# Optimization experiments

Measured on AMD Instinct MI355X. Metric: run time of the kernel, lower is better.

Reference implementation:

```python
import jax, jax.numpy as jnp
import numpy as np

B, S, D = 4, 2048, 1024
H = 16
HD = D // H  # head_dim = 64


def setup_inputs() -> dict:
    key = jax.random.key(0)
    ks = jax.random.split(key, 8)
    scale = 1.0 / np.sqrt(D)
    return {
        "X_Q": jax.random.normal(ks[0], (B, S, D), dtype=jnp.float32),
        "X_KV": jax.random.normal(ks[1], (B, S, D), dtype=jnp.float32),
        # q_proj: Linear(D, D), weights stored as (in, out)
        "q_w": jax.random.normal(ks[2], (D, D), dtype=jnp.float32) * scale,
        "q_b": jax.random.normal(ks[3], (D,), dtype=jnp.float32) * scale,
        # kv_proj: Linear(D, 2*D)
        "kv_w": jax.random.normal(ks[4], (D, 2 * D), dtype=jnp.float32) * scale,
        "kv_b": jax.random.normal(ks[5], (2 * D,), dtype=jnp.float32) * scale,
        # out_proj: Linear(D, D) (query_dim == input_dim)
        "out_w": jax.random.normal(ks[6], (D, D), dtype=jnp.float32) * scale,
        "out_b": jax.random.normal(ks[7], (D,), dtype=jnp.float32) * scale,
    }


def reference(X_Q, X_KV, q_w, q_b, kv_w, kv_b, out_w, out_b):
    # projections
    q = X_Q @ q_w + q_b                      # [b, s, D]
    kv = X_KV @ kv_w + kv_b                  # [b, l, 2D]
    k, v = jnp.split(kv, 2, axis=-1)         # each [b, l, D]

    def split_heads(t):
        b, m, _ = t.shape
        return t.reshape(b, m, H, HD).transpose(0, 2, 1, 3)  # [b, h, m, d]

    q, k, v = split_heads(q), split_heads(k), split_heads(v)

    # standard attention: full SxL scores (non-flash path)
    scores = jnp.einsum("bhsd,bhld->bhsl", q, k) / np.sqrt(HD)
    attn = jax.nn.softmax(scores, axis=-1)   # dropout_p = 0 -> identity
    out = jnp.einsum("bhsl,bhld->bhsd", attn, v)

    # merge heads: [b, h, s, d] -> [b, s, h*d]
    out = out.transpose(0, 2, 1, 3).reshape(B, S, D)
    return out @ out_w + out_b
```

## Files before the change

### kernel.cpp

```cpp
#include <hip/hip_runtime.h>
#include <hip/hip_bf16.h>
#include <math.h>

#define B_  4
#define S_  2048
#define D_  1024
#define H_  16
#define HD_ 64

typedef __bf16 bf16;
typedef __bf16 bf16x4 __attribute__((ext_vector_type(4)));
typedef __bf16 bf16x8 __attribute__((ext_vector_type(8)));
typedef float  floatx4 __attribute__((ext_vector_type(4)));
typedef unsigned short ushort8 __attribute__((ext_vector_type(8)));

#define QSCALE 0.18033688011112042f

__device__ __forceinline__ void async_load16(const bf16* g, bf16* l) {
  __builtin_amdgcn_global_load_lds(
      (const __attribute__((address_space(1))) void*)g,
      (__attribute__((address_space(3))) void*)l, 16, 0, 0);
}

__global__ __launch_bounds__(256) void cast_both(
    const float* __restrict__ ina, bf16* __restrict__ outa,
    const float* __restrict__ inb, bf16* __restrict__ outb) {
  int bid = blockIdx.x;
  const float* in;
  bf16* out;
  int i;
  if (bid < 8192) { in = ina; out = outa; i = (bid * 256 + threadIdx.x) * 4; }
  else            { in = inb; out = outb; i = ((bid - 8192) * 256 + threadIdx.x) * 4; }
  float4 v = *reinterpret_cast<const float4*>(in + i);
  bf16x4 o;
  o[0] = (bf16)v.x; o[1] = (bf16)v.y; o[2] = (bf16)v.z; o[3] = (bf16)v.w;
  *reinterpret_cast<bf16x4*>(out + i) = o;
}

__global__ __launch_bounds__(256) void transcast_all(
    const float* __restrict__ qw, bf16* __restrict__ qwT,
    const float* __restrict__ kvw, bf16* __restrict__ kvwT,
    const float* __restrict__ ow, bf16* __restrict__ owT) {
  __shared__ float tile[32][33];
  int bid = blockIdx.x;
  const float* in; bf16* out; int N, lb;
  if (bid < 1024)      { in = qw;  out = qwT;  N = 1024; lb = bid; }
  else if (bid < 3072) { in = kvw; out = kvwT; N = 2048; lb = bid - 1024; }
  else                 { in = ow;  out = owT;  N = 1024; lb = bid - 3072; }
  int nx = N >> 5;
  int n0 = (lb % nx) * 32, k0 = (lb / nx) * 32;
  int tx = threadIdx.x & 31, ty = threadIdx.x >> 5;
  #pragma unroll
  for (int i = ty; i < 32; i += 8)
    tile[i][tx] = in[(size_t)(k0 + i) * N + n0 + tx];
  __syncthreads();
  #pragma unroll
  for (int i = ty; i < 32; i += 8)
    out[(size_t)(n0 + i) * 1024 + k0 + tx] = (bf16)tile[tx][i];
}

template <int MODE>
__global__ __launch_bounds__(256) void gemm_bt(
    const bf16* __restrict__ A, const bf16* __restrict__ Bt,
    const float* __restrict__ bias, void* __restrict__ out,
    int M, int N, int K) {
  __shared__ bf16 As[128][64];
  __shared__ bf16 Bs[128][64];

  const int tid  = threadIdx.x;
  const int m0   = blockIdx.y * 128;
  const int n0   = blockIdx.x * 128;
  const int w    = tid >> 6;
  const int lane = tid & 63;
  const int lr   = lane & 15;
  const int lq   = lane >> 4;
  const int wm   = (w >> 1) * 64;
  const int wn   = (w & 1) * 64;

  const int srow = lane >> 3;
  const int sg   = (lane & 7) ^ srow;
  const bf16* aptr = A  + (size_t)(m0 + 32 * w + srow) * K + 8 * sg;
  const bf16* bptr = Bt + (size_t)(n0 + 32 * w + srow) * K + 8 * sg;

  floatx4 acc[4][4];
  #pragma unroll
  for (int i = 0; i < 4; i++)
    #pragma unroll
    for (int j = 0; j < 4; j++)
      acc[i][j] = floatx4{0.f, 0.f, 0.f, 0.f};

  for (int k0 = 0; k0 < K; k0 += 64) {
    __syncthreads();
    #pragma unroll
    for (int p = 0; p < 4; p++) {
      async_load16(aptr + (size_t)8 * p * K + k0, &As[32 * w + 8 * p][0]);
      async_load16(bptr + (size_t)8 * p * K + k0, &Bs[32 * w + 8 * p][0]);
    }
    __syncthreads();
    #pragma unroll
    for (int kc = 0; kc < 2; kc++) {
      const int sw = 8 * ((kc * 4 + lq) ^ (lr & 7));
      bf16x8 af[4], bfv[4];
      #pragma unroll
      for (int t = 0; t < 4; t++)
        af[t] = *reinterpret_cast<const bf16x8*>(&As[wm + 16 * t + lr][sw]);
      #pragma unroll
      for (int t = 0; t < 4; t++)
        bfv[t] = *reinterpret_cast<const bf16x8*>(&Bs[wn + 16 * t + lr][sw]);
      #pragma unroll
      for (int i = 0; i < 4; i++)
        #pragma unroll
        for (int j = 0; j < 4; j++)
          acc[i][j] = __builtin_amdgcn_mfma_f32_16x16x32_bf16(af[i], bfv[j], acc[i][j], 0, 0, 0);
    }
  }

  #pragma unroll
  for (int i = 0; i < 4; i++) {
    int row_base = m0 + wm + 16 * i + lq * 4;
    #pragma unroll
    for (int j = 0; j < 4; j++) {
      int col = n0 + wn + 16 * j + lr;
      float bv = bias[col];
      if (MODE == 2 && col >= 1024) {
        int b = row_base >> 11, s0 = row_base & 2047;
        int c = col - 1024, h = c >> 6, d = c & 63;
        bf16* Vt = (bf16*)out + (size_t)B_ * H_ * S_ * HD_;
        bf16x4 pk;
        #pragma unroll
        for (int r = 0; r < 4; r++) pk[r] = (bf16)(acc[i][j][r] + bv);
        *reinterpret_cast<bf16x4*>(
            &Vt[(((size_t)b * H_ + h) * HD_ + d) * S_ + s0]) = pk;
        continue;
      }
      #pragma unroll
      for (int r = 0; r < 4; r++) {
        int row = row_base + r;
        float v = acc[i][j][r] + bv;
        if (MODE == 0) {
          ((float*)out)[(size_t)row * N + col] = v;
        } else if (MODE == 1) {
          int b = row >> 11, s = row & 2047;
          int h = col >> 6, d = col & 63;
          ((bf16*)out)[(((size_t)b * H_ + h) * S_ + s) * HD_ + d] =
              (bf16)(v * QSCALE);
        } else {
          int b = row >> 11, s = row & 2047;
          int h = col >> 6, d = col & 63;
          ((bf16*)out)[(((size_t)b * H_ + h) * S_ + s) * HD_ + d] = (bf16)v;
        }
      }
    }
  }
}

__global__ __launch_bounds__(256, 2) void attn_kernel(
    const bf16* __restrict__ Q, const bf16* __restrict__ Kb,
    const bf16* __restrict__ Vt, bf16* __restrict__ out) {
  __shared__ bf16 smem[32768];

  const int tid  = threadIdx.x;
  const int w    = tid >> 6;
  const int lane = tid & 63;
  const int lr   = lane & 15;
  const int lq   = lane >> 4;
  const int bh   = blockIdx.x;
  const int q0   = blockIdx.y * 256;
  const size_t base = (size_t)bh * S_ * HD_;

  bf16* pw = smem + 16384 + w * 4096;

  const int srow = lane >> 3;
  const int sg   = (lane & 7) ^ srow;

  const bf16* kptr = Kb + base + (size_t)(16 * w + srow) * HD_ + 8 * sg;
  const bf16* vptr = Vt + base + (size_t)(16 * w + srow) * S_  + 8 * sg;

  #pragma unroll
  for (int p = 0; p < 2; p++) {
    async_load16(kptr + (size_t)8 * p * HD_, smem + (16 * w + 8 * p) * 64);
    async_load16(vptr + (size_t)8 * p * S_,  smem + 4096 + (16 * w + 8 * p) * 64);
  }

  bf16x8 bq[4][2];
  #pragma unroll
  for (int g = 0; g < 4; g++) {
    const bf16* qrow = Q + base + (size_t)(q0 + 64 * w + 16 * g + lr) * HD_;
    bq[g][0] = *reinterpret_cast<const bf16x8*>(qrow + lq * 8);
    bq[g][1] = *reinterpret_cast<const bf16x8*>(qrow + 32 + lq * 8);
  }

  const int sw0 = 8 * ((0 + lq) ^ (lr & 7));
  const int sw1 = 8 * ((4 + lq) ^ (lr & 7));
  const int pcolbase = 4 * (lq & 1);
  const int pswz = lr & 7;

  float l_i[4] = {0.f, 0.f, 0.f, 0.f};
  floatx4 o_acc[4][4];
  #pragma unroll
  for (int g = 0; g < 4; g++)
    #pragma unroll
    for (int t = 0; t < 4; t++) o_acc[g][t] = floatx4{0.f, 0.f, 0.f, 0.f};

  __syncthreads();

  const int NIT = S_ / 64;
  for (int it = 0; it < NIT; it++) {
    bf16* ks  = smem + (it & 1) * 8192;
    bf16* vts = ks + 4096;

    if (it + 1 < NIT) {
      bf16* ksn = smem + ((it + 1) & 1) * 8192;
      const int l0n = (it + 1) * 64;
      #pragma unroll
      for (int p = 0; p < 2; p++) {
        async_load16(kptr + (size_t)(l0n + 8 * p) * HD_, ksn + (16 * w + 8 * p) * 64);
        async_load16(vptr + (size_t)8 * p * S_ + l0n,    ksn + 4096 + (16 * w + 8 * p) * 64);
      }
    }

    auto qkt = [&](int t) {
      bf16x8 ak0 = *reinterpret_cast<const bf16x8*>(ks + (16 * t + lr) * 64 + sw0);
      bf16x8 ak1 = *reinterpret_cast<const bf16x8*>(ks + (16 * t + lr) * 64 + sw1);
      floatx4 sc[4];
      #pragma unroll
      for (int g = 0; g < 4; g++) {
        sc[g] = __builtin_amdgcn_mfma_f32_16x16x32_bf16(ak0, bq[g][0],
                    floatx4{0.f, 0.f, 0.f, 0.f}, 0, 0, 0);
        sc[g] = __builtin_amdgcn_mfma_f32_16x16x32_bf16(ak1, bq[g][1], sc[g], 0, 0, 0);
      }
      const int pcol = 8 * ((2 * t + (lq >> 1)) ^ pswz) + pcolbase;
      #pragma unroll
      for (int g = 0; g < 4; g++) {
        bf16x4 pk;
        float lsum = 0.f;
        #pragma unroll
        for (int r = 0; r < 4; r++) {
          float p = __builtin_amdgcn_exp2f(sc[g][r]);
          lsum += p;
          pk[r] = (bf16)p;
        }
        l_i[g] += lsum;
        *reinterpret_cast<bf16x4*>(&pw[(16 * g + lr) * 64 + pcol]) = pk;
      }
    };

    qkt(0);
    qkt(1);
    __builtin_amdgcn_wave_barrier();

    {
      bf16x8 bp0[4], av0[4];
      #pragma unroll
      for (int g = 0; g < 4; g++)
        bp0[g] = *reinterpret_cast<const bf16x8*>(&pw[(16 * g + lr) * 64 + sw0]);
      #pragma unroll
      for (int t2 = 0; t2 < 4; t2++)
        av0[t2] = *reinterpret_cast<const bf16x8*>(vts + (16 * t2 + lr) * 64 + sw0);
      qkt(2);
      #pragma unroll
      for (int t2 = 0; t2 < 2; t2++)
        #pragma unroll
        for (int g = 0; g < 4; g++)
          o_acc[g][t2] = __builtin_amdgcn_mfma_f32_16x16x32_bf16(av0[t2], bp0[g], o_acc[g][t2], 0, 0, 0);
      qkt(3);
      #pragma unroll
      for (int t2 = 2; t2 < 4; t2++)
        #pragma unroll
        for (int g = 0; g < 4; g++)
          o_acc[g][t2] = __builtin_amdgcn_mfma_f32_16x16x32_bf16(av0[t2], bp0[g], o_acc[g][t2], 0, 0, 0);
    }
    __builtin_amdgcn_wave_barrier();

    {
      bf16x8 bp1[4];
      #pragma unroll
      for (int g = 0; g < 4; g++)
        bp1[g] = *reinterpret_cast<const bf16x8*>(&pw[(16 * g + lr) * 64 + sw1]);
      #pragma unroll
      for (int t2 = 0; t2 < 4; t2++) {
        bf16x8 av = *reinterpret_cast<const bf16x8*>(vts + (16 * t2 + lr) * 64 + sw1);
        #pragma unroll
        for (int g = 0; g < 4; g++)
          o_acc[g][t2] = __builtin_amdgcn_mfma_f32_16x16x32_bf16(av, bp1[g], o_acc[g][t2], 0, 0, 0);
      }
    }

    __syncthreads();
  }

  #pragma unroll
  for (int g = 0; g < 4; g++) {
    l_i[g] += __shfl_xor(l_i[g], 16, 64);
    l_i[g] += __shfl_xor(l_i[g], 32, 64);
  }

  const int b = bh >> 4, h = bh & 15;
  #pragma unroll
  for (int g = 0; g < 4; g++) {
    const float inv = 1.0f / l_i[g];
    const int qrow = q0 + 64 * w + 16 * g + lr;
    bf16* orow = out + ((size_t)b * S_ + qrow) * D_ + h * HD_;
    #pragma unroll
    for (int t = 0; t < 4; t++) {
      bf16x4 pk;
      #pragma unroll
      for (int r = 0; r < 4; r++) pk[r] = (bf16)(o_acc[g][t][r] * inv);
      *reinterpret_cast<bf16x4*>(&orow[16 * t + lq * 4]) = pk;
    }
  }
}

extern "C" void kernel_launch(void* const* d_in, const int* in_sizes, int n_in,
                              void* d_out, int out_size, void* d_ws, size_t ws_size,
                              hipStream_t stream) {
  const float* X_Q   = (const float*)d_in[0];
  const float* X_KV  = (const float*)d_in[1];
  const float* q_w   = (const float*)d_in[2];
  const float* q_b   = (const float*)d_in[3];
  const float* kv_w  = (const float*)d_in[4];
  const float* kv_b  = (const float*)d_in[5];
  const float* out_w = (const float*)d_in[6];
  const float* out_b = (const float*)d_in[7];
  float* out = (float*)d_out;

  char* ws = (char*)d_ws;
  const size_t MB = 1024 * 1024;
  bf16* Xq   = (bf16*)(ws + 0);
  bf16* Xkv  = (bf16*)(ws + 16 * MB);
  bf16* Qb   = (bf16*)(ws + 32 * MB);
  bf16* Kb   = (bf16*)(ws + 48 * MB);
  bf16* qwT  = (bf16*)(ws + 80 * MB);
  bf16* kvwT = (bf16*)(ws + 82 * MB);
  bf16* owT  = (bf16*)(ws + 86 * MB);
  bf16* Vt   = Kb + (size_t)B_ * H_ * S_ * HD_;
  bf16* attn = Xq;

  cast_both<<<16384, 256, 0, stream>>>(X_Q, Xq, X_KV, Xkv);
  transcast_all<<<4096, 256, 0, stream>>>(q_w, qwT, kv_w, kvwT, out_w, owT);

  gemm_bt<1><<<dim3(8, 64), 256, 0, stream>>>(Xq, qwT, q_b, Qb, 8192, 1024, 1024);
  gemm_bt<2><<<dim3(16, 64), 256, 0, stream>>>(Xkv, kvwT, kv_b, Kb, 8192, 2048, 1024);
  attn_kernel<<<dim3(64, 8), 256, 0, stream>>>(Qb, Kb, Vt, attn);
  gemm_bt<0><<<dim3(8, 64), 256, 0, stream>>>(attn, owT, out_b, out, 8192, 1024, 1024);
}
```

Measured before the change: 308.5 us.

## Merge Q and KV projection GEMMs into one launch, add MFMA priority hints

Result: no change. 309.0 us (+0.2%).

```diff
diff --git a/kernel.cpp b/kernel.cpp
--- a/kernel.cpp
+++ b/kernel.cpp
@@ -12,7 +12,6 @@
 typedef __bf16 bf16x4 __attribute__((ext_vector_type(4)));
 typedef __bf16 bf16x8 __attribute__((ext_vector_type(8)));
 typedef float  floatx4 __attribute__((ext_vector_type(4)));
-typedef unsigned short ushort8 __attribute__((ext_vector_type(8)));
 
 #define QSCALE 0.18033688011112042f
 
@@ -60,16 +59,14 @@
 }
 
 template <int MODE>
-__global__ __launch_bounds__(256) void gemm_bt(
+__device__ __forceinline__ void gemm_body(
     const bf16* __restrict__ A, const bf16* __restrict__ Bt,
     const float* __restrict__ bias, void* __restrict__ out,
-    int M, int N, int K) {
-  __shared__ bf16 As[128][64];
-  __shared__ bf16 Bs[128][64];
-
+    int M, int N, int K, int bx, int by,
+    bf16 (*As)[64], bf16 (*Bs)[64]) {
   const int tid  = threadIdx.x;
-  const int m0   = blockIdx.y * 128;
-  const int n0   = blockIdx.x * 128;
+  const int m0   = by * 128;
+  const int n0   = bx * 128;
   const int w    = tid >> 6;
   const int lane = tid & 63;
   const int lr   = lane & 15;
@@ -154,6 +151,31 @@
   }
 }
 
+__global__ __launch_bounds__(256) void gemm_out(
+    const bf16* __restrict__ A, const bf16* __restrict__ Bt,
+    const float* __restrict__ bias, void* __restrict__ out,
+    int M, int N, int K) {
+  __shared__ bf16 As[128][64];
+  __shared__ bf16 Bs[128][64];
+  gemm_body<0>(A, Bt, bias, out, M, N, K, blockIdx.x, blockIdx.y, As, Bs);
+}
+
+__global__ __launch_bounds__(256) void gemm_qkv(
+    const bf16* __restrict__ Xq, const bf16* __restrict__ qwT,
+    const float* __restrict__ q_b, bf16* __restrict__ Qb,
+    const bf16* __restrict__ Xkv, const bf16* __restrict__ kvwT,
+    const float* __restrict__ kv_b, bf16* __restrict__ KVb) {
+  __shared__ bf16 As[128][64];
+  __shared__ bf16 Bs[128][64];
+  int bid = blockIdx.x;
+  if (bid < 512) {
+    gemm_body<1>(Xq, qwT, q_b, Qb, 8192, 1024, 1024, bid & 7, bid >> 3, As, Bs);
+  } else {
+    int b2 = bid - 512;
+    gemm_body<2>(Xkv, kvwT, kv_b, KVb, 8192, 2048, 1024, b2 & 15, b2 >> 4, As, Bs);
+  }
+}
+
 __global__ __launch_bounds__(256, 2) void attn_kernel(
     const bf16* __restrict__ Q, const bf16* __restrict__ Kb,
     const bf16* __restrict__ Vt, bf16* __restrict__ out) {
@@ -204,6 +226,9 @@
 
   __syncthreads();
 
+  const bf16* kpf = kptr + (size_t)64 * HD_;
+  const bf16* vpf = vptr + 64;
+
   const int NIT = S_ / 64;
   for (int it = 0; it < NIT; it++) {
     bf16* ks  = smem + (it & 1) * 8192;
@@ -211,11 +236,10 @@
 
     if (it + 1 < NIT) {
       bf16* ksn = smem + ((it + 1) & 1) * 8192;
-      const int l0n = (it + 1) * 64;
       #pragma unroll
       for (int p = 0; p < 2; p++) {
-        async_load16(kptr + (size_t)(l0n + 8 * p) * HD_, ksn + (16 * w + 8 * p) * 64);
-        async_load16(vptr + (size_t)8 * p * S_ + l0n,    ksn + 4096 + (16 * w + 8 * p) * 64);
+        async_load16(kpf + (size_t)8 * p * HD_, ksn + (16 * w + 8 * p) * 64);
+        async_load16(vpf + (size_t)8 * p * S_,  ksn + 4096 + (16 * w + 8 * p) * 64);
       }
     }
 
@@ -258,17 +282,21 @@
       for (int t2 = 0; t2 < 4; t2++)
         av0[t2] = *reinterpret_cast<const bf16x8*>(vts + (16 * t2 + lr) * 64 + sw0);
       qkt(2);
+      __builtin_amdgcn_s_setprio(1);
       #pragma unroll
       for (int t2 = 0; t2 < 2; t2++)
         #pragma unroll
         for (int g = 0; g < 4; g++)
           o_acc[g][t2] = __builtin_amdgcn_mfma_f32_16x16x32_bf16(av0[t2], bp0[g], o_acc[g][t2], 0, 0, 0);
+      __builtin_amdgcn_s_setprio(0);
       qkt(3);
+      __builtin_amdgcn_s_setprio(1);
       #pragma unroll
       for (int t2 = 2; t2 < 4; t2++)
         #pragma unroll
         for (int g = 0; g < 4; g++)
           o_acc[g][t2] = __builtin_amdgcn_mfma_f32_16x16x32_bf16(av0[t2], bp0[g], o_acc[g][t2], 0, 0, 0);
+      __builtin_amdgcn_s_setprio(0);
     }
     __builtin_amdgcn_wave_barrier();
 
@@ -277,6 +305,7 @@
       #pragma unroll
       for (int g = 0; g < 4; g++)
         bp1[g] = *reinterpret_cast<const bf16x8*>(&pw[(16 * g + lr) * 64 + sw1]);
+      __builtin_amdgcn_s_setprio(1);
       #pragma unroll
       for (int t2 = 0; t2 < 4; t2++) {
         bf16x8 av = *reinterpret_cast<const bf16x8*>(vts + (16 * t2 + lr) * 64 + sw1);
@@ -284,8 +313,11 @@
         for (int g = 0; g < 4; g++)
           o_acc[g][t2] = __builtin_amdgcn_mfma_f32_16x16x32_bf16(av, bp1[g], o_acc[g][t2], 0, 0, 0);
       }
-    }
-
+      __builtin_amdgcn_s_setprio(0);
+    }
+
+    kpf += (size_t)64 * HD_;
+    vpf += 64;
     __syncthreads();
   }
 
@@ -339,8 +371,7 @@
   cast_both<<<16384, 256, 0, stream>>>(X_Q, Xq, X_KV, Xkv);
   transcast_all<<<4096, 256, 0, stream>>>(q_w, qwT, kv_w, kvwT, out_w, owT);
 
-  gemm_bt<1><<<dim3(8, 64), 256, 0, stream>>>(Xq, qwT, q_b, Qb, 8192, 1024, 1024);
-  gemm_bt<2><<<dim3(16, 64), 256, 0, stream>>>(Xkv, kvwT, kv_b, Kb, 8192, 2048, 1024);
+  gemm_qkv<<<1536, 256, 0, stream>>>(Xq, qwT, q_b, Qb, Xkv, kvwT, kv_b, Kb);
   attn_kernel<<<dim3(64, 8), 256, 0, stream>>>(Qb, Kb, Vt, attn);
-  gemm_bt<0><<<dim3(8, 64), 256, 0, stream>>>(attn, owT, out_b, out, 8192, 1024, 1024);
-}
+  gemm_out<<<dim3(8, 64), 256, 0, stream>>>(attn, owT, out_b, out, 8192, 1024, 1024);
+}
```
